# Optimization experiments

Measured on AMD Instinct MI355X. Metric: run time of the kernel, lower is better.

Reference implementation:

```python
import jax, jax.numpy as jnp
import numpy as np
from jax import lax
from jax.scipy.special import logsumexp

LOG2PI = 1.8378770664093453

def _gauss_lp(x, mean, logvar):
    return -0.5 * ((x - mean) ** 2 * jnp.exp(-logvar) + logvar + LOG2PI)

def setup_inputs() -> dict:
    key = jax.random.key(0)
    ks = jax.random.split(key, 12)
    B, T, D, H, X, K, U = 32, 1024, 512, 512, 32, 8, 2
    s = 0.05
    return {
        'ys': jax.random.normal(ks[0], (B, T, D), jnp.float32),
        'us': jax.random.normal(ks[1], (B, T, U), jnp.float32),
        'eps': jax.random.normal(ks[2], (B, T, X), jnp.float32),
        'W1': jax.random.normal(ks[3], (D, H), jnp.float32) * s,
        'b1': jnp.zeros((H,), jnp.float32),
        'Wmu': jax.random.normal(ks[4], (H, X), jnp.float32) * s,
        'bmu': jnp.zeros((X,), jnp.float32),
        'Wlv': jax.random.normal(ks[5], (H, X), jnp.float32) * s,
        'blv': jnp.zeros((X,), jnp.float32),
        'Wz': jax.random.normal(ks[6], (X, K * K), jnp.float32) * s,
        'bz': jnp.zeros((K * K,), jnp.float32),
        'A': jax.random.normal(ks[7], (K, X, X), jnp.float32) * s,
        'Bu': jax.random.normal(ks[8], (K, U, X), jnp.float32) * s,
        'bx': jnp.zeros((K, X), jnp.float32),
        'x_logvar': jnp.zeros((K, X), jnp.float32),
        'x0_mean': jax.random.normal(ks[9], (K, X), jnp.float32) * s,
        'x0_logvar': jnp.zeros((K, X), jnp.float32),
        'C': jax.random.normal(ks[10], (X, D), jnp.float32) * s,
        'd': jnp.zeros((D,), jnp.float32),
        'y_logvar': jnp.zeros((D,), jnp.float32),
        'log_init_z': jnp.zeros((K,), jnp.float32),
    }

def _forward_backward(log_a, log_b, log_init):
    # log_a: [B,T,K,K] with log_a[:,t,j,k] = log p(z_t=j | z_{t-1}=k); log_b: [B,T,K]
    B, T, K = log_b.shape
    la = jnp.moveaxis(log_a[:, 1:], 1, 0)  # [T-1,B,K,K]
    lb = jnp.moveaxis(log_b[:, 1:], 1, 0)  # [T-1,B,K]
    a0 = log_init[None, :] + log_b[:, 0]
    c0 = logsumexp(a0, axis=-1)
    a0 = a0 - c0[:, None]
    def fstep(alpha, ab):
        la_t, lb_t = ab
        a = lb_t + logsumexp(la_t + alpha[:, None, :], axis=-1)
        c = logsumexp(a, axis=-1)
        an = a - c[:, None]
        return an, (an, c)
    _, (alphas, cs) = lax.scan(fstep, a0, (la, lb))
    log_px = c0 + jnp.sum(cs, axis=0)  # [B] log marginal likelihood
    fwd = jnp.concatenate([a0[None], alphas], axis=0)  # [T,B,K]
    betaT = jnp.zeros((B, K), log_b.dtype)
    def bstep(beta, ab):
        la_t, lb_t = ab
        b = logsumexp(la_t + (lb_t + beta)[:, :, None], axis=1)  # sum over next-state j
        b = b - logsumexp(b, axis=-1, keepdims=True)
        return b, b
    _, betas = lax.scan(bstep, betaT, (la, lb), reverse=True)
    bwd = jnp.concatenate([betas, betaT[None]], axis=0)  # [T,B,K]
    lg = fwd + bwd
    log_gamma1 = lg - logsumexp(lg, axis=-1, keepdims=True)
    return jnp.moveaxis(log_gamma1, 0, 1), log_px

def reference(ys, us, eps, W1, b1, Wmu, bmu, Wlv, blv, Wz, bz, A, Bu, bx,
              x_logvar, x0_mean, x0_logvar, C, d, y_logvar, log_init_z):
    B, T, D = ys.shape
    K, X = x0_mean.shape
    # inference net q(x|y): per-step MLP producing Gaussian, reparameterized sample
    h = jnp.tanh(ys @ W1 + b1)
    mu = h @ Wmu + bmu
    lv = h @ Wlv + blv
    x = mu + jnp.exp(0.5 * lv) * eps                        # [B,T,X]
    x_entropy = 0.5 * jnp.sum(eps ** 2 + lv + LOG2PI, -1)   # -log q(x^), [B,T]
    # discrete transition log p(z_t | z_{t-1}, x_{t-1}) with log(eye) prepended at t=0
    logits = (x[:, :-1] @ Wz + bz).reshape(B, T - 1, K, K)
    log_a_t = jax.nn.log_softmax(logits, axis=-2)           # normalize_logprob axis=-2
    log_eye = jnp.log(jnp.eye(K, dtype=ys.dtype) + 1e-10)[None, None]
    log_a = jnp.concatenate([jnp.broadcast_to(log_eye, (B, 1, K, K)), log_a_t], axis=1)
    # continuous likelihood log p(x_t | x_{t-1}, u_t, z_t=k) -> [B,T,K]
    log_b0 = jnp.sum(_gauss_lp(x[:, 0, None, :], x0_mean, x0_logvar), -1)  # [B,K]
    means = (jnp.einsum('btd,kde->btke', x[:, :-1], A)
             + jnp.einsum('btu,kue->btke', us[:, 1:], Bu) + bx)            # [B,T-1,K,X]
    log_bt = jnp.sum(_gauss_lp(x[:, 1:, None, :], means, x_logvar), -1)
    log_b = jnp.concatenate([log_b0[:, None], log_bt], axis=1)
    log_init = jax.nn.log_softmax(log_init_z)
    log_gamma1, log_px = _forward_backward(log_a, log_b, log_init)
    # posterior-weighted generated mean mixed over states, then emission
    xt1_gen = jnp.sum(means * jnp.exp(log_gamma1[:, 1:, :, None]), axis=-2)
    x_gen1 = jnp.concatenate([x[:, :1], xt1_gen], axis=1)
    y_mean = x_gen1 @ C + d
    log_py = jnp.sum(_gauss_lp(ys, y_mean, y_logvar), -1)   # [B,T]
    log_p_xy = log_px + jnp.sum(log_py, -1)                 # [B]
    log_qx = jnp.mean(jnp.sum(x_entropy, 1))
    elbo = jnp.mean(log_p_xy) + log_qx
    return elbo
```

## Files before the change

kernel.cpp:

```cpp
#include <hip/hip_runtime.h>
#include <math.h>

#define LOG2PI 1.8378770664093453f

#define NB 32
#define NT 1024
#define ND 512
#define NH 512
#define NX 32
#define NK 8
#define NU 2

#define NCH 93
#define CHL 11

typedef __attribute__((ext_vector_type(8))) short bf16x8;
typedef __attribute__((ext_vector_type(4))) float f32x4;

__device__ __forceinline__ unsigned short f2bf(float f) {
    unsigned u = __float_as_uint(f);
    unsigned r = (u + 0x7FFF + ((u >> 16) & 1)) >> 16;
    return (unsigned short)r;
}

__device__ __forceinline__ unsigned pack_bf2(float a, float b) {
    unsigned ua = __float_as_uint(a) + 0x8000u;
    unsigned ub = __float_as_uint(b) + 0x8000u;
    return __builtin_amdgcn_perm(ub, ua, 0x07060302);
}

#define DPP_X1 0xB1
#define DPP_X2 0x4E
#define DPP_X3 0x1B
#define DPP_X7 0x141

template <int CTRL>
__device__ __forceinline__ float dppx(float v) {
    return __int_as_float(__builtin_amdgcn_update_dpp(
        0, __float_as_int(v), CTRL, 0xF, 0xF, true));
}

__device__ __forceinline__ float fb_matvec(float4 a0, float4 a1, float v) {
    float p1 = dppx<DPP_X1>(v);
    float p2 = dppx<DPP_X2>(v);
    float p3 = dppx<DPP_X3>(v);
    float p7 = dppx<DPP_X7>(v);
    float p4 = dppx<DPP_X7>(p3);
    float p5 = dppx<DPP_X7>(p2);
    float p6 = dppx<DPP_X7>(p1);
    float c0 = fmaf(a0.y, p1, a0.x * v);
    float c1 = fmaf(a0.w, p3, a0.z * p2);
    float c2 = fmaf(a1.y, p5, a1.x * p4);
    float c3 = fmaf(a1.w, p7, a1.z * p6);
    return (c0 + c1) + (c2 + c3);
}

__device__ __forceinline__ float fb_matvecT(float4 a0, float4 a1, float w) {
    float q0 = a0.x * w;
    float t1 = dppx<DPP_X1>(a0.y * w);
    float t2 = dppx<DPP_X2>(a0.z * w);
    float t3 = dppx<DPP_X3>(a0.w * w);
    float t7 = dppx<DPP_X7>(a1.w * w);
    float t4 = dppx<DPP_X7>(dppx<DPP_X3>(a1.x * w));
    float t5 = dppx<DPP_X7>(dppx<DPP_X2>(a1.y * w));
    float t6 = dppx<DPP_X7>(dppx<DPP_X1>(a1.z * w));
    return ((q0 + t1) + (t2 + t3)) + ((t4 + t5) + (t6 + t7));
}

__device__ __forceinline__ float gsum8(float v) {
    float s = v + dppx<DPP_X1>(v);
    s = s + dppx<DPP_X2>(s);
    s = s + dppx<DPP_X7>(dppx<DPP_X3>(s));
    return s;
}

__device__ __forceinline__ float lse8_high(float v) {
    float m = v;
    m = fmaxf(m, __shfl_xor(m, 8, 64));
    m = fmaxf(m, __shfl_xor(m, 16, 64));
    m = fmaxf(m, __shfl_xor(m, 32, 64));
    float s = expf(v - m);
    s += __shfl_xor(s, 8, 64);
    s += __shfl_xor(s, 16, 64);
    s += __shfl_xor(s, 32, 64);
    return m + logf(s);
}

__global__ __launch_bounds__(256) void k_castT(
    const float* __restrict__ W, unsigned short* __restrict__ WT)
{
    __shared__ float tile[32][33];
    const int bx = blockIdx.x * 32;
    const int by = blockIdx.y * 32;
    const int tx = threadIdx.x & 31, ty = threadIdx.x >> 5;
    for (int i = ty; i < 32; i += 8)
        tile[i][tx] = W[(size_t)(bx + i) * 512 + by + tx];
    __syncthreads();
    for (int i = ty; i < 32; i += 8)
        WT[(size_t)(by + i) * 512 + bx + tx] = f2bf(tile[tx][i]);
}

__global__ __launch_bounds__(256) void k_cast_mulv(
    const float* __restrict__ Wmu, const float* __restrict__ Wlv,
    unsigned short* __restrict__ out)
{
    __shared__ float tile[32][33];
    const float* W = blockIdx.y ? Wlv : Wmu;
    const int base = blockIdx.y * 32;
    const int g = blockIdx.x;
    const int tx = threadIdx.x & 31, ty = threadIdx.x >> 5;
    for (int i = ty; i < 32; i += 8)
        tile[i][tx] = W[(size_t)(g * 32 + i) * 32 + tx];
    __syncthreads();
    for (int i = ty; i < 32; i += 8)
        out[(size_t)(base + i) * 512 + g * 32 + tx] = f2bf(tile[tx][i]);
}

__global__ __launch_bounds__(256) void k_prepc1(
    const float* __restrict__ ylv, float* __restrict__ ivbuf,
    float* __restrict__ term0)
{
    __shared__ float part[256];
    const int tid = threadIdx.x;
    float s = 0.f;
    for (int i = tid; i < 512; i += 256) {
        float lv = ylv[i];
        ivbuf[i] = expf(-lv);
        s += lv + LOG2PI;
    }
    part[tid] = s;
    __syncthreads();
    for (int st = 128; st; st >>= 1) {
        if (tid < st) part[tid] += part[tid + st];
        __syncthreads();
    }
    if (tid == 0) term0[0] = part[0];
}

__global__ __launch_bounds__(256) void k_prepc2(
    const float* __restrict__ C, const float* __restrict__ dvec,
    const float* __restrict__ ivbuf, unsigned short* __restrict__ W2bf,
    float* __restrict__ G, float* __restrict__ c2x)
{
    const int x = blockIdx.x;
    const int tid = threadIdx.x;
    if (x == 32) {
        for (int i = tid; i < 32 * 512; i += 256)
            W2bf[i] = f2bf(C[i] * ivbuf[i & 511]);
        return;
    }
    const int y = tid >> 3, seg = tid & 7;
    const float* Cx = &C[(size_t)x * 512];
    const float* Cy = &C[(size_t)y * 512];
    float p = 0.f;
    for (int j = 0; j < 64; ++j) {
        int dcol = seg * 64 + j;
        p = fmaf(Cx[dcol] * ivbuf[dcol], Cy[dcol], p);
    }
    p = gsum8(p);
    if (seg == 0) G[x * 33 + y] = p;
    if (tid < 8) {
        float q = 0.f;
        for (int j = 0; j < 64; ++j) {
            int dcol = tid * 64 + j;
            q = fmaf(Cx[dcol] * ivbuf[dcol], dvec[dcol], q);
        }
        q = gsum8(q);
        if (tid == 0) c2x[x] = q;
    }
}

__global__ __launch_bounds__(256) void k_cast_ys_t1(
    const float* __restrict__ ys, const float* __restrict__ dvec,
    const float* __restrict__ ivbuf, unsigned short* __restrict__ ysb,
    float* __restrict__ term1)
{
    const int tid = threadIdx.x;
    const int c8 = tid & 7;
    const int rbase = blockIdx.x * 128;
    float t1p[4] = {0.f, 0.f, 0.f, 0.f};
    for (int k0 = 0; k0 < 512; k0 += 64) {
        const float4 dv0 = *reinterpret_cast<const float4*>(&dvec[k0 + c8 * 8]);
        const float4 dv1 = *reinterpret_cast<const float4*>(&dvec[k0 + c8 * 8 + 4]);
        const float4 iv0 = *reinterpret_cast<const float4*>(&ivbuf[k0 + c8 * 8]);
        const float4 iv1 = *reinterpret_cast<const float4*>(&ivbuf[k0 + c8 * 8 + 4]);
#pragma unroll
        for (int r = 0; r < 4; ++r) {
            int row = rbase + (tid >> 3) + r * 32;
            const float4 f0 = *reinterpret_cast<const float4*>(
                &ys[(size_t)row * 512 + k0 + c8 * 8]);
            const float4 f1 = *reinterpret_cast<const float4*>(
                &ys[(size_t)row * 512 + k0 + c8 * 8 + 4]);
            float g0 = f0.x - dv0.x, g1 = f0.y - dv0.y;
            float g2 = f0.z - dv0.z, g3 = f0.w - dv0.w;
            float g4 = f1.x - dv1.x, g5 = f1.y - dv1.y;
            float g6 = f1.z - dv1.z, g7 = f1.w - dv1.w;
            t1p[r] += (g0 * g0 * iv0.x + g1 * g1 * iv0.y)
                    + (g2 * g2 * iv0.z + g3 * g3 * iv0.w)
                    + (g4 * g4 * iv1.x + g5 * g5 * iv1.y)
                    + (g6 * g6 * iv1.z + g7 * g7 * iv1.w);
            uint4 ua;
            ua.x = pack_bf2(f0.x, f0.y);
            ua.y = pack_bf2(f0.z, f0.w);
            ua.z = pack_bf2(f1.x, f1.y);
            ua.w = pack_bf2(f1.z, f1.w);
            *reinterpret_cast<uint4*>(&ysb[(size_t)row * 512 + k0 + c8 * 8]) = ua;
        }
    }
#pragma unroll
    for (int r = 0; r < 4; ++r) {
        float s = gsum8(t1p[r]);
        if ((tid & 7) == 0) term1[rbase + (tid >> 3) + r * 32] = s;
    }
}

__global__ __launch_bounds__(256) void k_gemm_h_mfma(
    const unsigned short* __restrict__ Abf,
    const unsigned short* __restrict__ Bbf,
    const float* __restrict__ b1, unsigned short* __restrict__ hb)
{
    __shared__ unsigned short As[128 * 64];
    __shared__ unsigned short Bs[128 * 64];
    const int tid = threadIdx.x;
    const int bm = blockIdx.x * 128;
    const int bn = blockIdx.y * 128;
    const int wid = tid >> 6, lane = tid & 63;
    const int wm = wid >> 1, wn = wid & 1;

    f32x4 acc[4][4];
#pragma unroll
    for (int m = 0; m < 4; ++m)
#pragma unroll
        for (int n = 0; n < 4; ++n)
            acc[m][n] = (f32x4){0.f, 0.f, 0.f, 0.f};

    for (int k0 = 0; k0 < 512; k0 += 64) {
#pragma unroll
        for (int r = 0; r < 4; ++r) {
            int l = tid + r * 256;
            int row = l >> 3, c8 = l & 7;
            int sidx = row * 8 + (c8 ^ (row & 7));
            uint4 va = *reinterpret_cast<const uint4*>(
                &Abf[(size_t)(bm + row) * 512 + k0 + c8 * 8]);
            *reinterpret_cast<uint4*>(&As[sidx * 8]) = va;
            uint4 vb = *reinterpret_cast<const uint4*>(
                &Bbf[(size_t)(bn + row) * 512 + k0 + c8 * 8]);
            *reinterpret_cast<uint4*>(&Bs[sidx * 8]) = vb;
        }
        __syncthreads();
#pragma unroll
        for (int kh = 0; kh < 2; ++kh) {
            bf16x8 af[4], bfr[4];
            const int c8r = kh * 4 + (lane >> 4);
#pragma unroll
            for (int m = 0; m < 4; ++m) {
                int rA = wm * 64 + m * 16 + (lane & 15);
                af[m] = *reinterpret_cast<bf16x8*>(
                    &As[rA * 64 + (c8r ^ (rA & 7)) * 8]);
            }
#pragma unroll
            for (int n = 0; n < 4; ++n) {
                int rB = wn * 64 + n * 16 + (lane & 15);
                bfr[n] = *reinterpret_cast<bf16x8*>(
                    &Bs[rB * 64 + (c8r ^ (rB & 7)) * 8]);
            }
#pragma unroll
            for (int m = 0; m < 4; ++m)
#pragma unroll
                for (int n = 0; n < 4; ++n)
                    acc[m][n] = __builtin_amdgcn_mfma_f32_16x16x32_bf16(
                        af[m], bfr[n], acc[m][n], 0, 0, 0);
        }
        __syncthreads();
    }
    float b1v[4];
#pragma unroll
    for (int n = 0; n < 4; ++n)
        b1v[n] = b1[bn + wn * 64 + n * 16 + (lane & 15)];
#pragma unroll
    for (int m = 0; m < 4; ++m) {
#pragma unroll
        for (int q = 0; q < 4; ++q) {
            int row = bm + wm * 64 + m * 16 + (lane >> 4) * 4 + q;
#pragma unroll
            for (int n = 0; n < 4; ++n) {
                int col = bn + wn * 64 + n * 16 + (lane & 15);
                hb[(size_t)row * 512 + col] = f2bf(tanhf(acc[m][n][q] + b1v[n]));
            }
        }
    }
}

__global__ __launch_bounds__(256) void k_mulv_mfma(
    const unsigned short* __restrict__ hbf,
    const unsigned short* __restrict__ Wt,
    const float* __restrict__ bmu, const float* __restrict__ blv,
    const float* __restrict__ eps,
    float* __restrict__ x, float* __restrict__ xent)
{
    __shared__ unsigned short As[128 * 64];
    __shared__ unsigned short Bs[64 * 64];
    const int tid = threadIdx.x;
    const int bm = blockIdx.x * 128;
    const int wid = tid >> 6, lane = tid & 63;
    f32x4 acc[2][4];
#pragma unroll
    for (int m = 0; m < 2; ++m)
#pragma unroll
        for (int n = 0; n < 4; ++n)
            acc[m][n] = (f32x4){0.f, 0.f, 0.f, 0.f};

    for (int k0 = 0; k0 < 512; k0 += 64) {
#pragma unroll
        for (int r = 0; r < 4; ++r) {
            int l = tid + r * 256, row = l >> 3, c8 = l & 7;
            int sidx = row * 8 + (c8 ^ (row & 7));
            uint4 v = *reinterpret_cast<const uint4*>(
                &hbf[(size_t)(bm + row) * 512 + k0 + c8 * 8]);
            *reinterpret_cast<uint4*>(&As[sidx * 8]) = v;
        }
#pragma unroll
        for (int r = 0; r < 2; ++r) {
            int l = tid + r * 256, row = l >> 3, c8 = l & 7;
            int sidx = row * 8 + (c8 ^ (row & 7));
            uint4 v = *reinterpret_cast<const uint4*>(
                &Wt[(size_t)row * 512 + k0 + c8 * 8]);
            *reinterpret_cast<uint4*>(&Bs[sidx * 8]) = v;
        }
        __syncthreads();
#pragma unroll
        for (int kh = 0; kh < 2; ++kh) {
            const int c8r = kh * 4 + (lane >> 4);
            bf16x8 af[2], bfr[4];
#pragma unroll
            for (int m = 0; m < 2; ++m) {
                int rA = wid * 32 + m * 16 + (lane & 15);
                af[m] = *reinterpret_cast<bf16x8*>(
                    &As[rA * 64 + (c8r ^ (rA & 7)) * 8]);
            }
#pragma unroll
            for (int n = 0; n < 4; ++n) {
                int rB = n * 16 + (lane & 15);
                bfr[n] = *reinterpret_cast<bf16x8*>(
                    &Bs[rB * 64 + (c8r ^ (rB & 7)) * 8]);
            }
#pragma unroll
            for (int m = 0; m < 2; ++m)
#pragma unroll
                for (int n = 0; n < 4; ++n)
                    acc[m][n] = __builtin_amdgcn_mfma_f32_16x16x32_bf16(
                        af[m], bfr[n], acc[m][n], 0, 0, 0);
        }
        __syncthreads();
    }
    const int o0 = lane & 15, o1 = 16 + (lane & 15);
    const float bm0 = bmu[o0], bm1 = bmu[o1];
    const float bl0 = blv[o0], bl1 = blv[o1];
#pragma unroll
    for (int m = 0; m < 2; ++m) {
#pragma unroll
        for (int q = 0; q < 4; ++q) {
            int row = bm + wid * 32 + m * 16 + (lane >> 4) * 4 + q;
            float mu0 = acc[m][0][q] + bm0;
            float mu1 = acc[m][1][q] + bm1;
            float lv0 = acc[m][2][q] + bl0;
            float lv1 = acc[m][3][q] + bl1;
            float e0 = eps[(size_t)row * 32 + o0];
            float e1 = eps[(size_t)row * 32 + o1];
            x[(size_t)row * 32 + o0] = mu0 + expf(0.5f * lv0) * e0;
            x[(size_t)row * 32 + o1] = mu1 + expf(0.5f * lv1) * e1;
            float pe = (e0 * e0 + lv0) + (e1 * e1 + lv1);
            pe += __shfl_xor(pe, 1, 64);
            pe += __shfl_xor(pe, 2, 64);
            pe += __shfl_xor(pe, 4, 64);
            pe += __shfl_xor(pe, 8, 64);
            if ((lane & 15) == 0)
                xent[row] = 0.5f * (pe + 32.f * LOG2PI);
        }
    }
}

__global__ __launch_bounds__(256) void k_proj(
    const unsigned short* __restrict__ ysb,
    const unsigned short* __restrict__ W2bf, float* __restrict__ proj)
{
    __shared__ unsigned short As[128 * 64];
    __shared__ unsigned short Bs[32 * 64];
    const int tid = threadIdx.x;
    const int bm = blockIdx.x * 128;
    const int wid = tid >> 6, lane = tid & 63;
    f32x4 acc[2][2];
#pragma unroll
    for (int m = 0; m < 2; ++m)
#pragma unroll
        for (int n = 0; n < 2; ++n)
            acc[m][n] = (f32x4){0.f, 0.f, 0.f, 0.f};

    for (int k0 = 0; k0 < 512; k0 += 64) {
#pragma unroll
        for (int r = 0; r < 4; ++r) {
            int l = tid + r * 256, row = l >> 3, c8 = l & 7;
            int sidx = row * 8 + (c8 ^ (row & 7));
            uint4 v = *reinterpret_cast<const uint4*>(
                &ysb[(size_t)(bm + row) * 512 + k0 + c8 * 8]);
            *reinterpret_cast<uint4*>(&As[sidx * 8]) = v;
        }
        {
            int row = tid >> 3, c8 = tid & 7;
            int sidx = row * 8 + (c8 ^ (row & 7));
            uint4 v = *reinterpret_cast<const uint4*>(
                &W2bf[(size_t)row * 512 + k0 + c8 * 8]);
            *reinterpret_cast<uint4*>(&Bs[sidx * 8]) = v;
        }
        __syncthreads();
#pragma unroll
        for (int kh = 0; kh < 2; ++kh) {
            const int c8r = kh * 4 + (lane >> 4);
            bf16x8 af[2], bfr[2];
#pragma unroll
            for (int m = 0; m < 2; ++m) {
                int rA = wid * 32 + m * 16 + (lane & 15);
                af[m] = *reinterpret_cast<bf16x8*>(
                    &As[rA * 64 + (c8r ^ (rA & 7)) * 8]);
            }
#pragma unroll
            for (int n = 0; n < 2; ++n) {
                int rB = n * 16 + (lane & 15);
                bfr[n] = *reinterpret_cast<bf16x8*>(
                    &Bs[rB * 64 + (c8r ^ (rB & 7)) * 8]);
            }
#pragma unroll
            for (int m = 0; m < 2; ++m)
#pragma unroll
                for (int n = 0; n < 2; ++n)
                    acc[m][n] = __builtin_amdgcn_mfma_f32_16x16x32_bf16(
                        af[m], bfr[n], acc[m][n], 0, 0, 0);
        }
        __syncthreads();
    }
#pragma unroll
    for (int m = 0; m < 2; ++m)
#pragma unroll
        for (int q = 0; q < 4; ++q) {
            int row = bm + wid * 32 + m * 16 + (lane >> 4) * 4 + q;
#pragma unroll
            for (int n = 0; n < 2; ++n) {
                int col = n * 16 + (lane & 15);
                proj[(size_t)row * 32 + col] = acc[m][n][q];
            }
        }
}

__global__ __launch_bounds__(256) void k_loga(
    const float* __restrict__ x, const float* __restrict__ Wz,
    const float* __restrict__ bz, float* __restrict__ ap1)
{
    const int tid = threadIdx.x;
    const int item = blockIdx.x * 4 + (tid >> 6);
    const int lane = tid & 63;
    const int t = item & (NT - 1);
    if (t == 0) return;
    const int j = lane >> 3, k = lane & 7;
    const float* xr = &x[((size_t)item - 1) * 32];
    float acc = bz[lane];
#pragma unroll
    for (int e = 0; e < 32; ++e) acc = fmaf(xr[e], Wz[e * 64 + lane], acc);
    float lse = lse8_high(acc);
    ap1[(size_t)item * 64 + j * 8 + (j ^ k)] = expf(acc - lse);
}

__global__ __launch_bounds__(256) void k_means8(
    const float* __restrict__ x, const float* __restrict__ us,
    const float* __restrict__ A, const float* __restrict__ Bu,
    const float* __restrict__ bx, const float* __restrict__ x_logvar,
    float* __restrict__ log_b)
{
    __shared__ float As[8192];
    __shared__ float xs8[8][32];
    __shared__ float us8[8][2];
    const int tid = threadIdx.x;
    const int base = blockIdx.x * 8;
    for (int i = tid; i < 2048; i += 256)
        reinterpret_cast<float4*>(As)[i] =
            reinterpret_cast<const float4*>(A)[i];
    {
        int row = tid >> 5, xo = tid & 31;
        int item = base + row;
        int b = item / 1023, tm = item - b * 1023;
        xs8[row][xo] = x[((size_t)b * NT + tm) * 32 + xo];
        if (xo < 2) us8[row][xo] = us[((size_t)b * NT + tm + 1) * 2 + xo];
    }
    __syncthreads();
    const int k = tid >> 5, xo = tid & 31;
    const float bxv = bx[k * 32 + xo];
    const float bu0 = Bu[(k * 2 + 0) * 32 + xo];
    const float bu1 = Bu[(k * 2 + 1) * 32 + xo];
    const float lvv = x_logvar[k * 32 + xo];
    const float ivv = expf(-lvv);
    const float basev = lvv + LOG2PI;
    for (int i = 0; i < 8; ++i) {
        int item = base + i;
        int b = item / 1023, tm = item - b * 1023;
        float acc = fmaf(us8[i][0], bu0, fmaf(us8[i][1], bu1, bxv));
#pragma unroll 8
        for (int e = 0; e < 32; ++e)
            acc = fmaf(xs8[i][e], As[k * 1024 + e * 32 + xo], acc);
        float xv = x[((size_t)b * NT + tm + 1) * 32 + xo];
        float dd = xv - acc;
        float term = dd * dd * ivv + basev;
        for (int m = 16; m; m >>= 1) term += __shfl_down(term, m, 32);
        if (xo == 0)
            log_b[((size_t)b * NT + tm + 1) * 8 + k] = -0.5f * term;
    }
}

__global__ __launch_bounds__(256) void k_logb0(
    const float* __restrict__ x, const float* __restrict__ x0_mean,
    const float* __restrict__ x0_logvar, float* __restrict__ log_b)
{
    const int b = blockIdx.x;
    const int tid = threadIdx.x;
    const int k = tid >> 5, xo = tid & 31;
    float xv = x[((size_t)b * NT) * 32 + xo];
    float mm = x0_mean[k * 32 + xo];
    float lvv = x0_logvar[k * 32 + xo];
    float dd = xv - mm;
    float term = -0.5f * (dd * dd * expf(-lvv) + lvv + LOG2PI);
    for (int m = 16; m; m >>= 1) term += __shfl_down(term, m, 32);
    if (xo == 0) log_b[(size_t)b * NT * 8 + k] = term;
}

__global__ __launch_bounds__(256) void k_prep(
    const float* __restrict__ log_b, float* __restrict__ bexp,
    float* __restrict__ mbsum)
{
    __shared__ float part[256];
    const int b = blockIdx.x;
    const int tid = threadIdx.x;
    float msum = 0.f;
    for (int t = tid; t < NT; t += 256) {
        const float* lbp = &log_b[((size_t)b * NT + t) * 8];
        float4 l0 = *reinterpret_cast<const float4*>(lbp);
        float4 l1 = *reinterpret_cast<const float4*>(lbp + 4);
        float mm = fmaxf(fmaxf(fmaxf(l0.x, l0.y), fmaxf(l0.z, l0.w)),
                         fmaxf(fmaxf(l1.x, l1.y), fmaxf(l1.z, l1.w)));
        float4 e0, e1;
        e0.x = expf(l0.x - mm); e0.y = expf(l0.y - mm);
        e0.z = expf(l0.z - mm); e0.w = expf(l0.w - mm);
        e1.x = expf(l1.x - mm); e1.y = expf(l1.y - mm);
        e1.z = expf(l1.z - mm); e1.w = expf(l1.w - mm);
        float* bp = &bexp[((size_t)b * NT + t) * 8];
        *reinterpret_cast<float4*>(bp) = e0;
        *reinterpret_cast<float4*>(bp + 4) = e1;
        msum += mm;
    }
    part[tid] = msum;
    __syncthreads();
    for (int s = 128; s; s >>= 1) {
        if (tid < s) part[tid] += part[tid + s];
        __syncthreads();
    }
    if (tid == 0) mbsum[b] = part[0];
}

__global__ __launch_bounds__(256) void k_fbA(
    const float* __restrict__ ap1, const float* __restrict__ bexp,
    float* __restrict__ Pfx, float* __restrict__ sA)
{
    const int tid = threadIdx.x;
    const int wg = blockIdx.x * 4 + (tid >> 6);
    const int lane = tid & 63;
    const int b = wg / NCH;
    const int c = wg - b * NCH;
    const int j = lane >> 3, k = lane & 7;
    const float* ap = &ap1[(size_t)b * NT * 64];
    const float* be = &bexp[(size_t)b * NT * 8];
    int t = CHL * c + 1;
    float P = be[t * 8 + j] * ap[t * 64 + j * 8 + (j ^ k)];
    float sacc = 0.f;
    for (int i = 1; i < CHL; ++i) {
        ++t;
        float4 m0 = *reinterpret_cast<const float4*>(&ap[(size_t)t * 64 + j * 8]);
        float4 m1 = *reinterpret_cast<const float4*>(&ap[(size_t)t * 64 + j * 8 + 4]);
        float bj = be[(size_t)t * 8 + j];
        float x1 = __shfl_xor(P, 8, 64);
        float x2 = __shfl_xor(P, 16, 64);
        float x3 = __shfl_xor(P, 24, 64);
        float x4 = __shfl_xor(P, 32, 64);
        float x5 = __shfl_xor(P, 40, 64);
        float x6 = __shfl_xor(P, 48, 64);
        float x7 = __shfl_xor(P, 56, 64);
        float c0 = fmaf(m0.y, x1, m0.x * P);
        float c1 = fmaf(m0.w, x3, m0.z * x2);
        float c2 = fmaf(m1.y, x5, m1.x * x4);
        float c3 = fmaf(m1.w, x7, m1.z * x6);
        P = bj * ((c0 + c1) + (c2 + c3));
        if ((i & 3) == 3) {
            float mx = P;
            mx = fmaxf(mx, __shfl_xor(mx, 1, 64));
            mx = fmaxf(mx, __shfl_xor(mx, 2, 64));
            mx = fmaxf(mx, __shfl_xor(mx, 4, 64));
            mx = fmaxf(mx, __shfl_xor(mx, 8, 64));
            mx = fmaxf(mx, __shfl_xor(mx, 16, 64));
            mx = fmaxf(mx, __shfl_xor(mx, 32, 64));
            mx = fmaxf(mx, 1e-30f);
            float r = __builtin_amdgcn_rcpf(mx);
            P *= r;
            sacc -= __logf(r);
        }
    }
    Pfx[((size_t)b * NCH + c) * 64 + j * 8 + (j ^ k)] = P;
    if (lane == 0) sA[b * NCH + c] = sacc;
}

__global__ __launch_bounds__(128) void k_fbB(
    const float* __restrict__ Pfx, const float* __restrict__ sA,
    const float* __restrict__ bexp, const float* __restrict__ mbsum,
    const float* __restrict__ log_init_z,
    float* __restrict__ alphaB, float* __restrict__ betaB,
    float* __restrict__ log_px)
{
    const int b = blockIdx.x;
    const int tid = threadIdx.x;
    const int wave = tid >> 6;
    const int lane = tid & 63;
    const int st = lane & 7;
    const float* pf = &Pfx[(size_t)b * NCH * 64];
    if (wave == 0) {
        float liv[8];
        float mz = -1e30f, sz = 0.f;
#pragma unroll
        for (int q = 0; q < 8; ++q) liv[q] = log_init_z[q];
#pragma unroll
        for (int q = 0; q < 8; ++q) mz = fmaxf(mz, liv[q]);
#pragma unroll
        for (int q = 0; q < 8; ++q) sz += expf(liv[q] - mz);
        float alpha = (expf(liv[st] - mz) / sz) * bexp[(size_t)b * NT * 8 + st];
        float logS = 0.f, sAsum = 0.f;
        {
            float s = fmaxf(gsum8(alpha), 1e-35f);
            logS += __logf(s);
            alpha *= __builtin_amdgcn_rcpf(s);
        }
        if (lane < 8) alphaB[((size_t)b * (NCH + 1)) * 8 + lane] = alpha;
        for (int c = 0; c < NCH; ++c) {
            float4 a0 = *reinterpret_cast<const float4*>(&pf[(size_t)c * 64 + st * 8]);
            float4 a1 = *reinterpret_cast<const float4*>(&pf[(size_t)c * 64 + st * 8 + 4]);
            alpha = fb_matvec(a0, a1, alpha);
            float s = fmaxf(gsum8(alpha), 1e-35f);
            logS += __logf(s);
            alpha *= __builtin_amdgcn_rcpf(s);
            sAsum += sA[b * NCH + c];
            if (lane < 8) alphaB[((size_t)b * (NCH + 1) + c + 1) * 8 + lane] = alpha;
        }
        if (lane == 0) log_px[b] = mbsum[b] + sAsum + logS;
    } else {
        float beta = 1.f;
        if (lane < 8) betaB[((size_t)b * (NCH + 1) + NCH) * 8 + lane] = 1.f;
        for (int c = NCH - 1; c >= 0; --c) {
            float4 a0 = *reinterpret_cast<const float4*>(&pf[(size_t)c * 64 + st * 8]);
            float4 a1 = *reinterpret_cast<const float4*>(&pf[(size_t)c * 64 + st * 8 + 4]);
            beta = fb_matvecT(a0, a1, beta);
            float s = fmaxf(gsum8(beta), 1e-35f);
            beta *= __builtin_amdgcn_rcpf(s);
            if (lane < 8) betaB[((size_t)b * (NCH + 1) + c) * 8 + lane] = beta;
        }
    }
}

__global__ __launch_bounds__(256) void k_fbC(
    const float* __restrict__ ap1, const float* __restrict__ bexp,
    const float* __restrict__ alphaB, const float* __restrict__ betaB,
    float* __restrict__ gamma)
{
    __shared__ float alphaS[32][CHL][8];
    const int tid = threadIdx.x;
    const int g = tid >> 3;
    const int st = tid & 7;
    const int task = blockIdx.x * 32 + g;
    const int b = task / NCH;
    const int c = task - b * NCH;
    const float* ap = &ap1[(size_t)b * NT * 64];
    const float* be = &bexp[(size_t)b * NT * 8];
    const int t0 = CHL * c;
    float alpha = alphaB[((size_t)b * (NCH + 1) + c) * 8 + st];
#pragma unroll
    for (int i = 1; i <= CHL; ++i) {
        int t = t0 + i;
        float4 a0 = *reinterpret_cast<const float4*>(&ap[(size_t)t * 64 + st * 8]);
        float4 a1 = *reinterpret_cast<const float4*>(&ap[(size_t)t * 64 + st * 8 + 4]);
        float bv = be[(size_t)t * 8 + st];
        alpha = fb_matvec(a0, a1, alpha) * bv;
        if (i == 5)
            alpha *= __builtin_amdgcn_rcpf(fmaxf(gsum8(alpha), 1e-35f));
        alphaS[g][i - 1][st] = alpha;
    }
    float beta = betaB[((size_t)b * (NCH + 1) + c + 1) * 8 + st];
#pragma unroll
    for (int i = CHL; i >= 1; --i) {
        int t = t0 + i;
        float gv = alphaS[g][i - 1][st] * beta;
        float s = fmaxf(gsum8(gv), 1e-35f);
        gamma[((size_t)b * NT + t) * 8 + st] = gv * __builtin_amdgcn_rcpf(s);
        float4 a0 = *reinterpret_cast<const float4*>(&ap[(size_t)t * 64 + st * 8]);
        float4 a1 = *reinterpret_cast<const float4*>(&ap[(size_t)t * 64 + st * 8 + 4]);
        float bv = be[(size_t)t * 8 + st];
        beta = fb_matvecT(a0, a1, beta * bv);
        if (i == 6)
            beta *= __builtin_amdgcn_rcpf(fmaxf(gsum8(beta), 1e-35f));
    }
    if (c == 0) {
        float a0v = alphaB[((size_t)b * (NCH + 1)) * 8 + st];
        float gv = a0v * beta;
        float s = fmaxf(gsum8(gv), 1e-35f);
        gamma[((size_t)b * NT) * 8 + st] = gv * __builtin_amdgcn_rcpf(s);
    }
}

__global__ __launch_bounds__(256) void k_py(
    const float* __restrict__ x, const float* __restrict__ us,
    const float* __restrict__ A, const float* __restrict__ Bu,
    const float* __restrict__ bx, const float* __restrict__ gamma,
    const float* __restrict__ proj, const float* __restrict__ term1,
    const float* __restrict__ Gm, const float* __restrict__ c2x,
    const float* __restrict__ term0, const float* __restrict__ xent,
    float* __restrict__ red)
{
    __shared__ float As[8192];
    __shared__ float Gs[32 * 33];
    __shared__ float c2s[32];
    __shared__ float xp8[8][32];
    __shared__ float gs[8][8];
    __shared__ float us8[8][2];
    __shared__ float xgS[8][32];
    const int tid = threadIdx.x;
    const int itemBase = blockIdx.x * 8;
    const int t0 = itemBase & (NT - 1);
    for (int i = tid; i < 2048; i += 256)
        reinterpret_cast<float4*>(As)[i] =
            reinterpret_cast<const float4*>(A)[i];
    for (int i = tid; i < 32 * 33; i += 256) Gs[i] = Gm[i];
    if (tid < 32) c2s[tid] = c2x[tid];
    {
        int it = tid >> 5, xo = tid & 31;
        int t = t0 + it;
        int item = itemBase + it;
        xp8[it][xo] = (t > 0) ? x[((size_t)item - 1) * 32 + xo] : 0.f;
        if (xo < 8) gs[it][xo] = (t > 0) ? gamma[(size_t)item * 8 + xo] : 0.f;
        if (xo < 2) us8[it][xo] = (t > 0) ? us[(size_t)item * 2 + xo] : 0.f;
    }
    __syncthreads();
    const int it = tid >> 5;
    const int xo = tid & 31;
    const int t = t0 + it;
    const int item = itemBase + it;
    float xg;
    if (t == 0) {
        xg = x[(size_t)item * 32 + xo];
    } else {
        xg = 0.f;
#pragma unroll
        for (int k = 0; k < 8; ++k) {
            float acc = bx[k * 32 + xo];
            acc = fmaf(us8[it][0], Bu[(k * 2 + 0) * 32 + xo], acc);
            acc = fmaf(us8[it][1], Bu[(k * 2 + 1) * 32 + xo], acc);
#pragma unroll 8
            for (int e = 0; e < 32; ++e)
                acc = fmaf(xp8[it][e], As[k * 1024 + e * 32 + xo], acc);
            xg = fmaf(gs[it][k], acc, xg);
        }
    }
    xgS[it][xo] = xg;
    __syncthreads();
    float gmv = 0.f;
#pragma unroll 8
    for (int y = 0; y < 32; ++y)
        gmv = fmaf(Gs[xo * 33 + y], xgS[it][y], gmv);
    float val = xg * (proj[(size_t)item * 32 + xo] - c2s[xo] - 0.5f * gmv);
    val += __shfl_xor(val, 1, 64);
    val += __shfl_xor(val, 2, 64);
    val += __shfl_xor(val, 4, 64);
    val += __shfl_xor(val, 8, 64);
    val += __shfl_xor(val, 16, 64);
    if (xo == 0)
        red[item] = -0.5f * (term1[item] + term0[0]) + val + xent[item];
}

__global__ __launch_bounds__(256) void k_final(
    const float* __restrict__ red, const float* __restrict__ log_px,
    float* __restrict__ out)
{
    __shared__ float ssum[4];
    float s = 0.f;
    for (int i = threadIdx.x; i < NB * NT; i += 256) s += red[i];
    if (threadIdx.x < NB) s += log_px[threadIdx.x];
#pragma unroll
    for (int m = 1; m < 64; m <<= 1) s += __shfl_xor(s, m, 64);
    if ((threadIdx.x & 63) == 0) ssum[threadIdx.x >> 6] = s;
    __syncthreads();
    if (threadIdx.x == 0)
        out[0] = (ssum[0] + ssum[1] + ssum[2] + ssum[3]) / (float)NB;
}

extern "C" void kernel_launch(void* const* d_in, const int* in_sizes, int n_in,
                              void* d_out, int out_size, void* d_ws,
                              size_t ws_size, hipStream_t stream)
{
    const float* ys        = (const float*)d_in[0];
    const float* us        = (const float*)d_in[1];
    const float* eps       = (const float*)d_in[2];
    const float* W1        = (const float*)d_in[3];
    const float* b1        = (const float*)d_in[4];
    const float* Wmu       = (const float*)d_in[5];
    const float* bmu       = (const float*)d_in[6];
    const float* Wlv       = (const float*)d_in[7];
    const float* blv       = (const float*)d_in[8];
    const float* Wz        = (const float*)d_in[9];
    const float* bz        = (const float*)d_in[10];
    const float* A         = (const float*)d_in[11];
    const float* Bu        = (const float*)d_in[12];
    const float* bx        = (const float*)d_in[13];
    const float* x_logvar  = (const float*)d_in[14];
    const float* x0_mean   = (const float*)d_in[15];
    const float* x0_logvar = (const float*)d_in[16];
    const float* C         = (const float*)d_in[17];
    const float* dv        = (const float*)d_in[18];
    const float* y_logvar  = (const float*)d_in[19];
    const float* log_init_z= (const float*)d_in[20];
    float* out = (float*)d_out;

    float* ws = (float*)d_ws;
    float* hbf_f  = ws;
    float* x      = hbf_f + 8388608;
    float* xent   = x + 1048576;
    float* ap1    = xent + 32768;
    float* bexp   = ap1 + 2097152;
    float* log_b  = bexp + 262144;
    float* ysb_f  = log_b + 262144;
    float* gam    = ysb_f + 8388608;
    float* log_px = gam + 262144;
    float* mbsum  = log_px + 32;
    float* red    = mbsum + 32;
    float* w1t_f  = red + 32768;
    float* wmlv_f = w1t_f + 131072;
    float* proj   = wmlv_f + 16384;
    float* term1  = proj + 1048576;
    float* ivbuf  = term1 + 32768;
    float* w2bf_f = ivbuf + 512;
    float* Gm     = w2bf_f + 8192;
    float* c2x    = Gm + 1056;
    float* term0  = c2x + 32;
    float* Pfx    = term0 + 1;
    float* sA     = Pfx + 190464;
    float* alphaB = sA + 2976;
    float* betaB  = alphaB + 24064;

    unsigned short* hbf  = (unsigned short*)hbf_f;
    unsigned short* ysb  = (unsigned short*)ysb_f;
    unsigned short* w1t  = (unsigned short*)w1t_f;
    unsigned short* wmlv = (unsigned short*)wmlv_f;
    unsigned short* w2bf = (unsigned short*)w2bf_f;

    k_prepc1   <<<1, 256, 0, stream>>>(y_logvar, ivbuf, term0);
    k_cast_ys_t1<<<256, 256, 0, stream>>>(ys, dv, ivbuf, ysb, term1);
    k_castT    <<<dim3(16, 16), 256, 0, stream>>>(W1, w1t);
    k_cast_mulv<<<dim3(16, 2), 256, 0, stream>>>(Wmu, Wlv, wmlv);
    k_prepc2   <<<33, 256, 0, stream>>>(C, dv, ivbuf, w2bf, Gm, c2x);
    k_gemm_h_mfma<<<dim3(256, 4), 256, 0, stream>>>(ysb, w1t, b1, hbf);
    k_proj     <<<256, 256, 0, stream>>>(ysb, w2bf, proj);
    k_mulv_mfma<<<256, 256, 0, stream>>>(hbf, wmlv, bmu, blv, eps, x, xent);
    k_loga     <<<8192, 256, 0, stream>>>(x, Wz, bz, ap1);
    k_means8   <<<4092, 256, 0, stream>>>(x, us, A, Bu, bx, x_logvar, log_b);
    k_logb0    <<<32, 256, 0, stream>>>(x, x0_mean, x0_logvar, log_b);
    k_prep     <<<32, 256, 0, stream>>>(log_b, bexp, mbsum);
    k_fbA      <<<744, 256, 0, stream>>>(ap1, bexp, Pfx, sA);
    k_fbB      <<<32, 128, 0, stream>>>(Pfx, sA, bexp, mbsum, log_init_z,
                                        alphaB, betaB, log_px);
    k_fbC      <<<93, 256, 0, stream>>>(ap1, bexp, alphaB, betaB, gam);
    k_py       <<<4096, 256, 0, stream>>>(x, us, A, Bu, bx, gam, proj, term1,
                                          Gm, c2x, term0, xent, red);
    k_final    <<<1, 256, 0, stream>>>(red, log_px, out);
}
```

Before: 283.0 us.

## Fuse hidden GEMM, mu/logvar GEMM and projection into one MLP kernel

Merges the h=tanh(ys·W1) GEMM, the mu/logvar GEMM and the ys·W2 projection into a single kernel that keeps each 64-row hidden tile in shared memory as bf16 instead of writing the full hidden matrix to global memory and reading it back. This removes a large intermediate buffer and two launches. In exchange, W1 tiles are now reloaded by every 64-row block, and Wt/W2 operands are read straight from global memory inside the MFMA loops. Separately, k_loga is restructured to stage 32 rows of x in shared memory and keep Wz columns in registers, and precise exp/log/tanh are swapped for fast intrinsics.

```diff
diff --git a/kernel.cpp b/kernel.cpp
--- a/kernel.cpp
+++ b/kernel.cpp
@@ -27,6 +27,11 @@
     unsigned ua = __float_as_uint(a) + 0x8000u;
     unsigned ub = __float_as_uint(b) + 0x8000u;
     return __builtin_amdgcn_perm(ub, ua, 0x07060302);
+}
+
+__device__ __forceinline__ float tanh_fast(float v) {
+    float t = __expf(2.0f * v);
+    return 1.0f - 2.0f * __builtin_amdgcn_rcpf(t + 1.0f);
 }
 
 #define DPP_X1 0xB1
@@ -79,11 +84,11 @@
     m = fmaxf(m, __shfl_xor(m, 8, 64));
     m = fmaxf(m, __shfl_xor(m, 16, 64));
     m = fmaxf(m, __shfl_xor(m, 32, 64));
-    float s = expf(v - m);
+    float s = __expf(v - m);
     s += __shfl_xor(s, 8, 64);
     s += __shfl_xor(s, 16, 64);
     s += __shfl_xor(s, 32, 64);
-    return m + logf(s);
+    return m + __logf(s);
 }
 
 __global__ __launch_bounds__(256) void k_castT(
@@ -214,259 +219,195 @@
     }
 }
 
-__global__ __launch_bounds__(256) void k_gemm_h_mfma(
-    const unsigned short* __restrict__ Abf,
-    const unsigned short* __restrict__ Bbf,
-    const float* __restrict__ b1, unsigned short* __restrict__ hb)
-{
-    __shared__ unsigned short As[128 * 64];
-    __shared__ unsigned short Bs[128 * 64];
-    const int tid = threadIdx.x;
-    const int bm = blockIdx.x * 128;
-    const int bn = blockIdx.y * 128;
+__global__ __launch_bounds__(256) void k_mlp(
+    const unsigned short* __restrict__ ysb,
+    const unsigned short* __restrict__ W1T,
+    const unsigned short* __restrict__ Wt,
+    const unsigned short* __restrict__ W2bf,
+    const float* __restrict__ b1,
+    const float* __restrict__ bmu, const float* __restrict__ blv,
+    const float* __restrict__ eps,
+    float* __restrict__ x, float* __restrict__ xent,
+    float* __restrict__ proj)
+{
+    __shared__ unsigned short SMEM[12288];
+    unsigned short* As = SMEM;
+    unsigned short* Bs = SMEM + 4096;
+    const int tid = threadIdx.x;
+    const int bm = blockIdx.x * 64;
     const int wid = tid >> 6, lane = tid & 63;
     const int wm = wid >> 1, wn = wid & 1;
-
-    f32x4 acc[4][4];
-#pragma unroll
-    for (int m = 0; m < 4; ++m)
+    const int l15 = lane & 15, l16 = lane >> 4;
+
+    f32x4 acc_mv[4];
+    f32x4 acc_pj[2];
+#pragma unroll
+    for (int n = 0; n < 4; ++n) acc_mv[n] = (f32x4){0.f, 0.f, 0.f, 0.f};
+#pragma unroll
+    for (int n = 0; n < 2; ++n) acc_pj[n] = (f32x4){0.f, 0.f, 0.f, 0.f};
+
+    for (int s = 0; s < 4; ++s) {
+        const int bn = s * 128;
+        f32x4 acc_h[2][4];
+#pragma unroll
+        for (int m = 0; m < 2; ++m)
+#pragma unroll
+            for (int n = 0; n < 4; ++n)
+                acc_h[m][n] = (f32x4){0.f, 0.f, 0.f, 0.f};
+
+        for (int k0 = 0; k0 < 512; k0 += 64) {
+#pragma unroll
+            for (int r = 0; r < 2; ++r) {
+                int l = tid + r * 256;
+                int row = l >> 3, c8 = l & 7;
+                int sidx = row * 8 + (c8 ^ (row & 7));
+                uint4 va = *reinterpret_cast<const uint4*>(
+                    &ysb[(size_t)(bm + row) * 512 + k0 + c8 * 8]);
+                *reinterpret_cast<uint4*>(&As[sidx * 8]) = va;
+            }
+#pragma unroll
+            for (int r = 0; r < 4; ++r) {
+                int l = tid + r * 256;
+                int row = l >> 3, c8 = l & 7;
+                int sidx = row * 8 + (c8 ^ (row & 7));
+                uint4 vb = *reinterpret_cast<const uint4*>(
+                    &W1T[(size_t)(bn + row) * 512 + k0 + c8 * 8]);
+                *reinterpret_cast<uint4*>(&Bs[sidx * 8]) = vb;
+            }
+            __syncthreads();
+#pragma unroll
+            for (int kh = 0; kh < 2; ++kh) {
+                const int c8r = kh * 4 + l16;
+                bf16x8 af[2], bfr[4];
+#pragma unroll
+                for (int m = 0; m < 2; ++m) {
+                    int rA = wm * 32 + m * 16 + l15;
+                    af[m] = *reinterpret_cast<bf16x8*>(
+                        &As[rA * 64 + (c8r ^ (rA & 7)) * 8]);
+                }
+#pragma unroll
+                for (int n = 0; n < 4; ++n) {
+                    int rB = wn * 64 + n * 16 + l15;
+                    bfr[n] = *reinterpret_cast<bf16x8*>(
+                        &Bs[rB * 64 + (c8r ^ (rB & 7)) * 8]);
+                }
+#pragma unroll
+                for (int m = 0; m < 2; ++m)
+#pragma unroll
+                    for (int n = 0; n < 4; ++n)
+                        acc_h[m][n] = __builtin_amdgcn_mfma_f32_16x16x32_bf16(
+                            af[m], bfr[n], acc_h[m][n], 0, 0, 0);
+                if (s == 0) {
+#pragma unroll
+                    for (int n2 = 0; n2 < 2; ++n2) {
+                        bf16x8 b2 = *reinterpret_cast<const bf16x8*>(
+                            &W2bf[(size_t)(n2 * 16 + l15) * 512 + k0 + c8r * 8]);
+                        acc_pj[n2] = __builtin_amdgcn_mfma_f32_16x16x32_bf16(
+                            af[wn], b2, acc_pj[n2], 0, 0, 0);
+                    }
+                }
+            }
+            __syncthreads();
+        }
+        float b1v[4];
 #pragma unroll
         for (int n = 0; n < 4; ++n)
-            acc[m][n] = (f32x4){0.f, 0.f, 0.f, 0.f};
-
-    for (int k0 = 0; k0 < 512; k0 += 64) {
-#pragma unroll
-        for (int r = 0; r < 4; ++r) {
-            int l = tid + r * 256;
-            int row = l >> 3, c8 = l & 7;
-            int sidx = row * 8 + (c8 ^ (row & 7));
-            uint4 va = *reinterpret_cast<const uint4*>(
-                &Abf[(size_t)(bm + row) * 512 + k0 + c8 * 8]);
-            *reinterpret_cast<uint4*>(&As[sidx * 8]) = va;
-            uint4 vb = *reinterpret_cast<const uint4*>(
-                &Bbf[(size_t)(bn + row) * 512 + k0 + c8 * 8]);
-            *reinterpret_cast<uint4*>(&Bs[sidx * 8]) = vb;
+            b1v[n] = b1[bn + wn * 64 + n * 16 + l15];
+#pragma unroll
+        for (int m = 0; m < 2; ++m) {
+#pragma unroll
+            for (int q = 0; q < 4; ++q) {
+                int row = wm * 32 + m * 16 + l16 * 4 + q;
+#pragma unroll
+                for (int n = 0; n < 4; ++n) {
+                    int col = wn * 64 + n * 16 + l15;
+                    float hv = tanh_fast(acc_h[m][n][q] + b1v[n]);
+                    int slot = (col >> 3) ^ (row & 15);
+                    SMEM[row * 128 + slot * 8 + (col & 7)] = f2bf(hv);
+                }
+            }
         }
         __syncthreads();
 #pragma unroll
-        for (int kh = 0; kh < 2; ++kh) {
-            bf16x8 af[4], bfr[4];
-            const int c8r = kh * 4 + (lane >> 4);
-#pragma unroll
-            for (int m = 0; m < 4; ++m) {
-                int rA = wm * 64 + m * 16 + (lane & 15);
-                af[m] = *reinterpret_cast<bf16x8*>(
-                    &As[rA * 64 + (c8r ^ (rA & 7)) * 8]);
+        for (int kh = 0; kh < 4; ++kh) {
+            const int c8r = kh * 4 + l16;
+            int rA = wid * 16 + l15;
+            bf16x8 af2 = *reinterpret_cast<bf16x8*>(
+                &SMEM[rA * 128 + (c8r ^ (rA & 15)) * 8]);
+            bf16x8 bf2[4];
+#pragma unroll
+            for (int n = 0; n < 4; ++n) {
+                int rB = n * 16 + l15;
+                bf2[n] = *reinterpret_cast<const bf16x8*>(
+                    &Wt[(size_t)rB * 512 + bn + c8r * 8]);
             }
 #pragma unroll
-            for (int n = 0; n < 4; ++n) {
-                int rB = wn * 64 + n * 16 + (lane & 15);
-                bfr[n] = *reinterpret_cast<bf16x8*>(
-                    &Bs[rB * 64 + (c8r ^ (rB & 7)) * 8]);
-            }
-#pragma unroll
-            for (int m = 0; m < 4; ++m)
-#pragma unroll
-                for (int n = 0; n < 4; ++n)
-                    acc[m][n] = __builtin_amdgcn_mfma_f32_16x16x32_bf16(
-                        af[m], bfr[n], acc[m][n], 0, 0, 0);
+            for (int n = 0; n < 4; ++n)
+                acc_mv[n] = __builtin_amdgcn_mfma_f32_16x16x32_bf16(
+                    af2, bf2[n], acc_mv[n], 0, 0, 0);
         }
         __syncthreads();
     }
-    float b1v[4];
-#pragma unroll
-    for (int n = 0; n < 4; ++n)
-        b1v[n] = b1[bn + wn * 64 + n * 16 + (lane & 15)];
-#pragma unroll
-    for (int m = 0; m < 4; ++m) {
-#pragma unroll
-        for (int q = 0; q < 4; ++q) {
-            int row = bm + wm * 64 + m * 16 + (lane >> 4) * 4 + q;
-#pragma unroll
-            for (int n = 0; n < 4; ++n) {
-                int col = bn + wn * 64 + n * 16 + (lane & 15);
-                hb[(size_t)row * 512 + col] = f2bf(tanhf(acc[m][n][q] + b1v[n]));
-            }
-        }
-    }
-}
-
-__global__ __launch_bounds__(256) void k_mulv_mfma(
-    const unsigned short* __restrict__ hbf,
-    const unsigned short* __restrict__ Wt,
-    const float* __restrict__ bmu, const float* __restrict__ blv,
-    const float* __restrict__ eps,
-    float* __restrict__ x, float* __restrict__ xent)
-{
-    __shared__ unsigned short As[128 * 64];
-    __shared__ unsigned short Bs[64 * 64];
-    const int tid = threadIdx.x;
-    const int bm = blockIdx.x * 128;
-    const int wid = tid >> 6, lane = tid & 63;
-    f32x4 acc[2][4];
-#pragma unroll
-    for (int m = 0; m < 2; ++m)
-#pragma unroll
-        for (int n = 0; n < 4; ++n)
-            acc[m][n] = (f32x4){0.f, 0.f, 0.f, 0.f};
-
-    for (int k0 = 0; k0 < 512; k0 += 64) {
-#pragma unroll
-        for (int r = 0; r < 4; ++r) {
-            int l = tid + r * 256, row = l >> 3, c8 = l & 7;
-            int sidx = row * 8 + (c8 ^ (row & 7));
-            uint4 v = *reinterpret_cast<const uint4*>(
-                &hbf[(size_t)(bm + row) * 512 + k0 + c8 * 8]);
-            *reinterpret_cast<uint4*>(&As[sidx * 8]) = v;
-        }
-#pragma unroll
-        for (int r = 0; r < 2; ++r) {
-            int l = tid + r * 256, row = l >> 3, c8 = l & 7;
-            int sidx = row * 8 + (c8 ^ (row & 7));
-            uint4 v = *reinterpret_cast<const uint4*>(
-                &Wt[(size_t)row * 512 + k0 + c8 * 8]);
-            *reinterpret_cast<uint4*>(&Bs[sidx * 8]) = v;
-        }
-        __syncthreads();
-#pragma unroll
-        for (int kh = 0; kh < 2; ++kh) {
-            const int c8r = kh * 4 + (lane >> 4);
-            bf16x8 af[2], bfr[4];
-#pragma unroll
-            for (int m = 0; m < 2; ++m) {
-                int rA = wid * 32 + m * 16 + (lane & 15);
-                af[m] = *reinterpret_cast<bf16x8*>(
-                    &As[rA * 64 + (c8r ^ (rA & 7)) * 8]);
-            }
-#pragma unroll
-            for (int n = 0; n < 4; ++n) {
-                int rB = n * 16 + (lane & 15);
-                bfr[n] = *reinterpret_cast<bf16x8*>(
-                    &Bs[rB * 64 + (c8r ^ (rB & 7)) * 8]);
-            }
-#pragma unroll
-            for (int m = 0; m < 2; ++m)
-#pragma unroll
-                for (int n = 0; n < 4; ++n)
-                    acc[m][n] = __builtin_amdgcn_mfma_f32_16x16x32_bf16(
-                        af[m], bfr[n], acc[m][n], 0, 0, 0);
-        }
-        __syncthreads();
-    }
-    const int o0 = lane & 15, o1 = 16 + (lane & 15);
+#pragma unroll
+    for (int q = 0; q < 4; ++q) {
+        int row = bm + wm * 32 + wn * 16 + l16 * 4 + q;
+        proj[(size_t)row * 32 + l15] = acc_pj[0][q];
+        proj[(size_t)row * 32 + 16 + l15] = acc_pj[1][q];
+    }
+    const int o0 = l15, o1 = 16 + l15;
     const float bm0 = bmu[o0], bm1 = bmu[o1];
     const float bl0 = blv[o0], bl1 = blv[o1];
 #pragma unroll
-    for (int m = 0; m < 2; ++m) {
-#pragma unroll
-        for (int q = 0; q < 4; ++q) {
-            int row = bm + wid * 32 + m * 16 + (lane >> 4) * 4 + q;
-            float mu0 = acc[m][0][q] + bm0;
-            float mu1 = acc[m][1][q] + bm1;
-            float lv0 = acc[m][2][q] + bl0;
-            float lv1 = acc[m][3][q] + bl1;
-            float e0 = eps[(size_t)row * 32 + o0];
-            float e1 = eps[(size_t)row * 32 + o1];
-            x[(size_t)row * 32 + o0] = mu0 + expf(0.5f * lv0) * e0;
-            x[(size_t)row * 32 + o1] = mu1 + expf(0.5f * lv1) * e1;
-            float pe = (e0 * e0 + lv0) + (e1 * e1 + lv1);
-            pe += __shfl_xor(pe, 1, 64);
-            pe += __shfl_xor(pe, 2, 64);
-            pe += __shfl_xor(pe, 4, 64);
-            pe += __shfl_xor(pe, 8, 64);
-            if ((lane & 15) == 0)
-                xent[row] = 0.5f * (pe + 32.f * LOG2PI);
-        }
-    }
-}
-
-__global__ __launch_bounds__(256) void k_proj(
-    const unsigned short* __restrict__ ysb,
-    const unsigned short* __restrict__ W2bf, float* __restrict__ proj)
-{
-    __shared__ unsigned short As[128 * 64];
-    __shared__ unsigned short Bs[32 * 64];
-    const int tid = threadIdx.x;
-    const int bm = blockIdx.x * 128;
-    const int wid = tid >> 6, lane = tid & 63;
-    f32x4 acc[2][2];
-#pragma unroll
-    for (int m = 0; m < 2; ++m)
-#pragma unroll
-        for (int n = 0; n < 2; ++n)
-            acc[m][n] = (f32x4){0.f, 0.f, 0.f, 0.f};
-
-    for (int k0 = 0; k0 < 512; k0 += 64) {
-#pragma unroll
-        for (int r = 0; r < 4; ++r) {
-            int l = tid + r * 256, row = l >> 3, c8 = l & 7;
-            int sidx = row * 8 + (c8 ^ (row & 7));
-            uint4 v = *reinterpret_cast<const uint4*>(
-                &ysb[(size_t)(bm + row) * 512 + k0 + c8 * 8]);
-            *reinterpret_cast<uint4*>(&As[sidx * 8]) = v;
-        }
-        {
-            int row = tid >> 3, c8 = tid & 7;
-            int sidx = row * 8 + (c8 ^ (row & 7));
-            uint4 v = *reinterpret_cast<const uint4*>(
-                &W2bf[(size_t)row * 512 + k0 + c8 * 8]);
-            *reinterpret_cast<uint4*>(&Bs[sidx * 8]) = v;
-        }
-        __syncthreads();
-#pragma unroll
-        for (int kh = 0; kh < 2; ++kh) {
-            const int c8r = kh * 4 + (lane >> 4);
-            bf16x8 af[2], bfr[2];
-#pragma unroll
-            for (int m = 0; m < 2; ++m) {
-                int rA = wid * 32 + m * 16 + (lane & 15);
-                af[m] = *reinterpret_cast<bf16x8*>(
-                    &As[rA * 64 + (c8r ^ (rA & 7)) * 8]);
-            }
-#pragma unroll
-            for (int n = 0; n < 2; ++n) {
-                int rB = n * 16 + (lane & 15);
-                bfr[n] = *reinterpret_cast<bf16x8*>(
-                    &Bs[rB * 64 + (c8r ^ (rB & 7)) * 8]);
-            }
-#pragma unroll
-            for (int m = 0; m < 2; ++m)
-#pragma unroll
-                for (int n = 0; n < 2; ++n)
-                    acc[m][n] = __builtin_amdgcn_mfma_f32_16x16x32_bf16(
-                        af[m], bfr[n], acc[m][n], 0, 0, 0);
-        }
-        __syncthreads();
-    }
-#pragma unroll
-    for (int m = 0; m < 2; ++m)
-#pragma unroll
-        for (int q = 0; q < 4; ++q) {
-            int row = bm + wid * 32 + m * 16 + (lane >> 4) * 4 + q;
-#pragma unroll
-            for (int n = 0; n < 2; ++n) {
-                int col = n * 16 + (lane & 15);
-                proj[(size_t)row * 32 + col] = acc[m][n][q];
-            }
-        }
+    for (int q = 0; q < 4; ++q) {
+        int row = bm + wid * 16 + l16 * 4 + q;
+        float mu0 = acc_mv[0][q] + bm0;
+        float mu1 = acc_mv[1][q] + bm1;
+        float lv0 = acc_mv[2][q] + bl0;
+        float lv1 = acc_mv[3][q] + bl1;
+        float e0 = eps[(size_t)row * 32 + o0];
+        float e1 = eps[(size_t)row * 32 + o1];
+        x[(size_t)row * 32 + o0] = mu0 + __expf(0.5f * lv0) * e0;
+        x[(size_t)row * 32 + o1] = mu1 + __expf(0.5f * lv1) * e1;
+        float pe = (e0 * e0 + lv0) + (e1 * e1 + lv1);
+        pe += __shfl_xor(pe, 1, 64);
+        pe += __shfl_xor(pe, 2, 64);
+        pe += __shfl_xor(pe, 4, 64);
+        pe += __shfl_xor(pe, 8, 64);
+        if (l15 == 0) xent[row] = 0.5f * (pe + 32.f * LOG2PI);
+    }
 }
 
 __global__ __launch_bounds__(256) void k_loga(
     const float* __restrict__ x, const float* __restrict__ Wz,
     const float* __restrict__ bz, float* __restrict__ ap1)
 {
-    const int tid = threadIdx.x;
-    const int item = blockIdx.x * 4 + (tid >> 6);
+    __shared__ float xs[32][32];
+    const int tid = threadIdx.x;
     const int lane = tid & 63;
-    const int t = item & (NT - 1);
-    if (t == 0) return;
+    const int wv = tid >> 6;
+    const int itemBase = blockIdx.x * 32;
+    {
+        int r = tid >> 3, cc = (tid & 7) * 4;
+        int item = itemBase + r;
+        int src = (item & (NT - 1)) ? item - 1 : item;
+        *reinterpret_cast<float4*>(&xs[r][cc]) =
+            *reinterpret_cast<const float4*>(&x[(size_t)src * 32 + cc]);
+    }
+    float wcol[32];
+#pragma unroll
+    for (int e = 0; e < 32; ++e) wcol[e] = Wz[e * 64 + lane];
+    const float bzv = bz[lane];
+    __syncthreads();
     const int j = lane >> 3, k = lane & 7;
-    const float* xr = &x[((size_t)item - 1) * 32];
-    float acc = bz[lane];
-#pragma unroll
-    for (int e = 0; e < 32; ++e) acc = fmaf(xr[e], Wz[e * 64 + lane], acc);
-    float lse = lse8_high(acc);
-    ap1[(size_t)item * 64 + j * 8 + (j ^ k)] = expf(acc - lse);
+    for (int i = wv; i < 32; i += 4) {
+        int item = itemBase + i;
+        if ((item & (NT - 1)) == 0) continue;
+        float acc = bzv;
+#pragma unroll
+        for (int e = 0; e < 32; ++e) acc = fmaf(xs[i][e], wcol[e], acc);
+        float lse = lse8_high(acc);
+        ap1[(size_t)item * 64 + j * 8 + (j ^ k)] = __expf(acc - lse);
+    }
 }
 
 __global__ __launch_bounds__(256) void k_means8(
@@ -830,8 +771,7 @@
     float* out = (float*)d_out;
 
     float* ws = (float*)d_ws;
-    float* hbf_f  = ws;
-    float* x      = hbf_f + 8388608;
+    float* x      = ws;
     float* xent   = x + 1048576;
     float* ap1    = xent + 32768;
     float* bexp   = ap1 + 2097152;
@@ -855,29 +795,27 @@
     float* alphaB = sA + 2976;
     float* betaB  = alphaB + 24064;
 
-    unsigned short* hbf  = (unsigned short*)hbf_f;
     unsigned short* ysb  = (unsigned short*)ysb_f;
     unsigned short* w1t  = (unsigned short*)w1t_f;
     unsigned short* wmlv = (unsigned short*)wmlv_f;
     unsigned short* w2bf = (unsigned short*)w2bf_f;
 
-    k_prepc1   <<<1, 256, 0, stream>>>(y_logvar, ivbuf, term0);
+    k_prepc1    <<<1, 256, 0, stream>>>(y_logvar, ivbuf, term0);
     k_cast_ys_t1<<<256, 256, 0, stream>>>(ys, dv, ivbuf, ysb, term1);
-    k_castT    <<<dim3(16, 16), 256, 0, stream>>>(W1, w1t);
-    k_cast_mulv<<<dim3(16, 2), 256, 0, stream>>>(Wmu, Wlv, wmlv);
-    k_prepc2   <<<33, 256, 0, stream>>>(C, dv, ivbuf, w2bf, Gm, c2x);
-    k_gemm_h_mfma<<<dim3(256, 4), 256, 0, stream>>>(ysb, w1t, b1, hbf);
-    k_proj     <<<256, 256, 0, stream>>>(ysb, w2bf, proj);
-    k_mulv_mfma<<<256, 256, 0, stream>>>(hbf, wmlv, bmu, blv, eps, x, xent);
-    k_loga     <<<8192, 256, 0, stream>>>(x, Wz, bz, ap1);
-    k_means8   <<<4092, 256, 0, stream>>>(x, us, A, Bu, bx, x_logvar, log_b);
-    k_logb0    <<<32, 256, 0, stream>>>(x, x0_mean, x0_logvar, log_b);
-    k_prep     <<<32, 256, 0, stream>>>(log_b, bexp, mbsum);
-    k_fbA      <<<744, 256, 0, stream>>>(ap1, bexp, Pfx, sA);
-    k_fbB      <<<32, 128, 0, stream>>>(Pfx, sA, bexp, mbsum, log_init_z,
-                                        alphaB, betaB, log_px);
-    k_fbC      <<<93, 256, 0, stream>>>(ap1, bexp, alphaB, betaB, gam);
-    k_py       <<<4096, 256, 0, stream>>>(x, us, A, Bu, bx, gam, proj, term1,
-                                          Gm, c2x, term0, xent, red);
-    k_final    <<<1, 256, 0, stream>>>(red, log_px, out);
-}
+    k_castT     <<<dim3(16, 16), 256, 0, stream>>>(W1, w1t);
+    k_cast_mulv <<<dim3(16, 2), 256, 0, stream>>>(Wmu, Wlv, wmlv);
+    k_prepc2    <<<33, 256, 0, stream>>>(C, dv, ivbuf, w2bf, Gm, c2x);
+    k_mlp       <<<512, 256, 0, stream>>>(ysb, w1t, wmlv, w2bf, b1, bmu, blv,
+                                          eps, x, xent, proj);
+    k_loga      <<<1024, 256, 0, stream>>>(x, Wz, bz, ap1);
+    k_means8    <<<4092, 256, 0, stream>>>(x, us, A, Bu, bx, x_logvar, log_b);
+    k_logb0     <<<32, 256, 0, stream>>>(x, x0_mean, x0_logvar, log_b);
+    k_prep      <<<32, 256, 0, stream>>>(log_b, bexp, mbsum);
+    k_fbA       <<<744, 256, 0, stream>>>(ap1, bexp, Pfx, sA);
+    k_fbB       <<<32, 128, 0, stream>>>(Pfx, sA, bexp, mbsum, log_init_z,
+                                         alphaB, betaB, log_px);
+    k_fbC       <<<93, 256, 0, stream>>>(ap1, bexp, alphaB, betaB, gam);
+    k_py        <<<4096, 256, 0, stream>>>(x, us, A, Bu, bx, gam, proj, term1,
+                                           Gm, c2x, term0, xent, red);
+    k_final     <<<1, 256, 0, stream>>>(red, log_px, out);
+}
```

Result: no change. 278.9 us (-1.4%).
